# Kernel tuning notes

Measured on AMD Instinct MI355X. Metric: run time of the kernel, lower is better.

Reference implementation:

```python
import jax, jax.numpy as jnp
import numpy as np

EMB_DIM = 1024
N_HEAD = 16
HEAD_DIM = EMB_DIM // N_HEAD


def setup_inputs() -> dict:
    key = jax.random.key(0)
    kx, kq, kk, kv, ko = jax.random.split(key, 5)
    B, S = 4, 2048
    x = jax.random.normal(kx, (B, S, EMB_DIM), dtype=jnp.float32)
    attention_mask = jnp.ones((B, S), dtype=jnp.int32)
    s = 1.0 / np.sqrt(EMB_DIM)
    w_q = jax.random.normal(kq, (EMB_DIM, EMB_DIM), dtype=jnp.float32) * s
    w_k = jax.random.normal(kk, (EMB_DIM, EMB_DIM), dtype=jnp.float32) * s
    w_v = jax.random.normal(kv, (EMB_DIM, EMB_DIM), dtype=jnp.float32) * s
    w_o = jax.random.normal(ko, (EMB_DIM, EMB_DIM), dtype=jnp.float32) * s
    return {"x": x, "attention_mask": attention_mask,
            "w_q": w_q, "w_k": w_k, "w_v": w_v, "w_o": w_o}


def reference(x, attention_mask, w_q, w_k, w_v, w_o):
    B, S, _ = x.shape
    scale = 1.0 / np.sqrt(HEAD_DIM)
    # projections; nn.Linear computes x @ W^T
    def split_heads(t):
        return t.reshape(B, S, N_HEAD, HEAD_DIM).transpose(0, 2, 1, 3)  # [B,H,S,D]
    q = split_heads(x @ w_q.T)
    k = split_heads(x @ w_k.T)
    v = split_heads(x @ w_v.T)
    scores = jnp.einsum('bhqd,bhkd->bhqk', q, k) * scale  # [B,H,S,S]
    pad_mask = (attention_mask == 0)[:, None, None, :]          # [B,1,1,S]
    causal = jnp.triu(jnp.ones((S, S), dtype=bool), k=1)[None, None]  # [1,1,S,S]
    combined = pad_mask | causal
    scores = jnp.where(combined, -jnp.inf, scores)
    attn = jax.nn.softmax(scores, axis=-1)
    out = jnp.einsum('bhqk,bhkd->bhqd', attn, v)
    out = out.transpose(0, 2, 1, 3).reshape(B, S, EMB_DIM)
    return out @ w_o.T
```

## Files before the change

### kernel.cpp

```cpp
#include <hip/hip_runtime.h>

typedef __bf16 bf16x8 __attribute__((ext_vector_type(8)));
typedef float f32x4 __attribute__((ext_vector_type(4)));

#define LOG2E 1.4426950408889634f
#define NEGC (-12.0f * LOG2E)

__device__ inline unsigned short f2bf(float f) {
  unsigned int u = __builtin_bit_cast(unsigned int, f);
  u += 0x7fff + ((u >> 16) & 1);
  return (unsigned short)(u >> 16);
}

__device__ inline void async16(const void* g, void* l) {
  __builtin_amdgcn_global_load_lds(
      (__attribute__((address_space(1))) void*)(g),
      (__attribute__((address_space(3))) void*)(l), 16, 0, 0);
}

__global__ __launch_bounds__(256) void cast_all(
    const float* __restrict__ x, const float* __restrict__ w0,
    const float* __restrict__ w1, const float* __restrict__ w2,
    const float* __restrict__ w3, unsigned short* __restrict__ xb,
    unsigned short* __restrict__ ob ) {
  int id = blockIdx.x;
  const float* in;
  unsigned short* out;
  int boff;
  if (id < 8192) { in = x; out = xb; boff = id; }
  else {
    int w = (id - 8192) >> 10; boff = (id - 8192) & 1023;
    switch (w) { case 0: in = w0; break; case 1: in = w1; break;
                 case 2: in = w2; break; default: in = w3; }
    out = ob + (long)w * 1048576;
  }
  int i = (boff * 256 + threadIdx.x) * 4;
  float4 v = *(const float4*)(in + i);
  ushort4 o;
  o.x = f2bf(v.x); o.y = f2bf(v.y); o.z = f2bf(v.z); o.w = f2bf(v.w);
  *(ushort4*)(out + i) = o;
}

#define BM 128
#define BN 128
#define BK 32

__global__ __launch_bounds__(256, 3) void gemm_bt(
    const unsigned short* __restrict__ A, const unsigned short* __restrict__ W,
    void* __restrict__ out, int M, int N, int K, int mode) {
  __shared__ unsigned short SM[BM * BK + BN * BK];
  unsigned short* As = SM;
  unsigned short* Ws = SM + BM * BK;
  int tid = threadIdx.x;
  int lane = tid & 63, wid = tid >> 6;
  int wm = wid >> 1, wn = wid & 1;
  int l15 = lane & 15, quad = lane >> 4;
  int m0 = (blockIdx.x & 63) * BM, n0 = (blockIdx.x >> 6) * BN;

  f32x4 acc[4][4] = {};

  int srow = tid >> 2;
  int scol = (tid & 3) * 8;
  const unsigned short* Ag = A + (long)(m0 + srow) * K + scol;
  const unsigned short* Wg = W + (long)(n0 + srow) * K + scol;
  char* AsB = (char*)As + wid * 1024;
  char* WsB = (char*)Ws + wid * 1024;

  for (int kt = 0; kt < K; kt += BK) {
    __syncthreads();
    async16(Ag + kt, AsB);
    async16(Ag + kt + (long)64 * K, AsB + 4096);
    async16(Wg + kt, WsB);
    async16(Wg + kt + (long)64 * K, WsB + 4096);
    __syncthreads();
    bf16x8 af[4], wf[4];
#pragma unroll
    for (int t = 0; t < 4; t++)
      af[t] = *(const bf16x8*)(As + (wm * 64 + t * 16 + l15) * BK + quad * 8);
#pragma unroll
    for (int t = 0; t < 4; t++)
      wf[t] = *(const bf16x8*)(Ws + (wn * 64 + t * 16 + l15) * BK + quad * 8);
#pragma unroll
    for (int i = 0; i < 4; i++)
#pragma unroll
      for (int j = 0; j < 4; j++)
        acc[i][j] = __builtin_amdgcn_mfma_f32_16x16x32_bf16(af[i], wf[j], acc[i][j], 0, 0, 0);
  }

  if (mode == 0) {
    float* Cf = (float*)out;
#pragma unroll
    for (int i = 0; i < 4; i++) {
      int row = m0 + wm * 64 + i * 16 + quad * 4;
#pragma unroll
      for (int j = 0; j < 4; j++) {
        int col = n0 + wn * 64 + j * 16 + l15;
#pragma unroll
        for (int r = 0; r < 4; r++)
          Cf[(long)(row + r) * N + col] = acc[i][j][r];
      }
    }
  } else {
    unsigned short* Cb = (unsigned short*)out;
    int which = n0 >> 10;
    if (which == 2) {
#pragma unroll
      for (int i = 0; i < 4; i++)
#pragma unroll
        for (int j = 0; j < 4; j++) {
          int m = m0 + wm * 64 + i * 16 + quad * 4;
          int n = n0 + wn * 64 + j * 16 + l15;
          int nn = n & 1023;
          int b = m >> 11, s = m & 2047;
          int h = nn >> 6, d = nn & 63;
          ushort4 pk;
          pk.x = f2bf(acc[i][j][0]); pk.y = f2bf(acc[i][j][1]);
          pk.z = f2bf(acc[i][j][2]); pk.w = f2bf(acc[i][j][3]);
          *(ushort4*)(&Cb[16777216 + (((long)((b * 16 + h) * 64 + d)) << 11) + s]) = pk;
        }
    } else {
      float scale = (which == 0) ? 0.125f : 1.0f;
      int h0 = (n0 & 1023) >> 6;
      unsigned short* Es = SM;
#pragma unroll
      for (int qr = 0; qr < 4; qr++) {
        __syncthreads();
        if (wm == (qr >> 1)) {
#pragma unroll
          for (int ii = 0; ii < 2; ii++) {
            int i = (qr & 1) * 2 + ii;
#pragma unroll
            for (int j = 0; j < 4; j++)
#pragma unroll
              for (int r = 0; r < 4; r++) {
                int rr = (i & 1) * 16 + quad * 4 + r;
                Es[rr * 136 + wn * 64 + j * 16 + l15] = f2bf(acc[i][j][r] * scale);
              }
          }
        }
        __syncthreads();
#pragma unroll
        for (int p = 0; p < 2; p++) {
          int pair = p * 32 + (tid >> 3);
          int rq = pair >> 1;
          int head = pair & 1, c8 = tid & 7;
          uint4 v = *(const uint4*)(&Es[rq * 136 + head * 64 + c8 * 8]);
          int m = m0 + qr * 32 + rq;
          int b = m >> 11, s = m & 2047;
          int h = h0 + head;
          long idx = (long)which * 8388608 +
                     ((long)((b * 16 + h) * 2048 + s)) * 64 + c8 * 8;
          *(uint4*)(&Cb[idx]) = v;
        }
      }
    }
  }
}

#define BQ 128
#define BKV 64
#define PSTR 76

__global__ __launch_bounds__(256, 3) void attn(
    const unsigned short* __restrict__ Q, const unsigned short* __restrict__ Kt,
    const unsigned short* __restrict__ VT, const int* __restrict__ am,
    unsigned short* __restrict__ O) {
  __shared__ unsigned short QPs[BQ * PSTR];
  __shared__ unsigned short Ks[2][BKV * PSTR];
  const int S = 2048, D = 64;
  int tid = threadIdx.x, lane = tid & 63, wid = tid >> 6;
  int l15 = lane & 15, quad = lane >> 4;

  int id = blockIdx.x;
  int s = id >> 8;
  int r = id & 255;
  int bh = r & 63;
  int c = r >> 6;
  int qt;
  switch (s) { case 0: qt = 15 - c; break; case 1: qt = 8 + c; break;
               case 2: qt = 7 - c; break; default: qt = c; }
  int q0 = qt * BQ;
  int b = bh >> 4, h = bh & 15;
  const unsigned short* Qg = Q + (long)bh * S * D;
  const unsigned short* Kg = Kt + (long)bh * S * D;
  const unsigned short* Vg = VT + (long)bh * D * S;
  const int* amg = am + b * S;

  int row0 = tid >> 3, col0 = (tid & 7) * 8;
  int row1 = 32 + (tid >> 3), col1 = col0;

#pragma unroll
  for (int rr = 0; rr < 4; rr++) {
    int cc = rr * 256 + tid;
    int row = cc >> 3, col = (cc & 7) * 8;
    *(uint4*)(&QPs[row * PSTR + col]) = *(const uint4*)(Qg + (long)(q0 + row) * D + col);
  }

  uint4 kreg0 = *(const uint4*)(Kg + (long)row0 * D + col0);
  uint4 kreg1 = *(const uint4*)(Kg + (long)row1 * D + col1);

  __syncthreads();
  bf16x8 qf[2][2];
#pragma unroll
  for (int i = 0; i < 2; i++)
#pragma unroll
    for (int kk = 0; kk < 2; kk++)
      qf[i][kk] = *(const bf16x8*)(&QPs[(wid * 32 + i * 16 + l15) * PSTR + kk * 32 + quad * 8]);

  *(uint4*)(&Ks[0][row0 * PSTR + col0]) = kreg0;
  *(uint4*)(&Ks[0][row1 * PSTR + col1]) = kreg1;
  kreg0 = *(const uint4*)(Kg + (long)(BKV + row0) * D + col0);
  kreg1 = *(const uint4*)(Kg + (long)(BKV + row1) * D + col1);
  __syncthreads();

  f32x4 o_acc[2][4] = {};
  float lsum[2][4] = {};

  int tFull = q0 >> 6;
  int nt = tFull + 2;
  for (int t = 0; t < nt; t++) {
    int s0 = t * BKV;
    int cur = t & 1, nxt = cur ^ 1;

    *(uint4*)(&Ks[nxt][row0 * PSTR + col0]) = kreg0;
    *(uint4*)(&Ks[nxt][row1 * PSTR + col1]) = kreg1;

    int mvj[4];
#pragma unroll
    for (int j = 0; j < 4; j++) mvj[j] = amg[s0 + j * 16 + l15];

    f32x4 sacc[2][4] = {};
#pragma unroll
    for (int kk = 0; kk < 2; kk++) {
      bf16x8 kf[4];
#pragma unroll
      for (int j = 0; j < 4; j++)
        kf[j] = *(const bf16x8*)(&Ks[cur][(j * 16 + l15) * PSTR + kk * 32 + quad * 8]);
      __builtin_amdgcn_s_setprio(1);
#pragma unroll
      for (int i = 0; i < 2; i++)
#pragma unroll
        for (int j = 0; j < 4; j++)
          sacc[i][j] = __builtin_amdgcn_mfma_f32_16x16x32_bf16(qf[i][kk], kf[j], sacc[i][j], 0, 0, 0);
      __builtin_amdgcn_s_setprio(0);
    }

    __syncthreads();

    {
      long s0n = (long)(t + 2) * BKV; if (s0n > S - BKV) s0n = S - BKV;
      kreg0 = *(const uint4*)(Kg + (s0n + row0) * D + col0);
      kreg1 = *(const uint4*)(Kg + (s0n + row1) * D + col1);
    }

    bf16x8 vf[2][4];
#pragma unroll
    for (int kk = 0; kk < 2; kk++)
#pragma unroll
      for (int j = 0; j < 4; j++)
        vf[kk][j] = *(const bf16x8*)(Vg + (long)(j * 16 + l15) * S + s0 + kk * 32 + quad * 8);

    float fb[4];
#pragma unroll
    for (int j = 0; j < 4; j++) fb[j] = mvj[j] ? NEGC : -1e38f;

    if (t < tFull) {
#pragma unroll
      for (int i = 0; i < 2; i++)
#pragma unroll
        for (int rr = 0; rr < 4; rr++) {
          int prow = (wid * 32 + i * 16 + quad * 4 + rr) * PSTR;
          float rs = 0.f;
#pragma unroll
          for (int j = 0; j < 4; j++) {
            float p = __builtin_amdgcn_exp2f(fmaf(sacc[i][j][rr], LOG2E, fb[j]));
            unsigned int u = __builtin_bit_cast(unsigned int, p);
            QPs[prow + j * 16 + l15] = (unsigned short)(u >> 16);
            rs += __builtin_bit_cast(float, u & 0xffff0000u);
          }
          lsum[i][rr] += rs;
        }
    } else {
#pragma unroll
      for (int i = 0; i < 2; i++)
#pragma unroll
        for (int rr = 0; rr < 4; rr++) {
          int row = q0 + wid * 32 + i * 16 + quad * 4 + rr;
          int prow = (wid * 32 + i * 16 + quad * 4 + rr) * PSTR;
          float rs = 0.f;
#pragma unroll
          for (int j = 0; j < 4; j++) {
            int col = s0 + j * 16 + l15;
            float fbe = (col > row) ? -1e38f : fb[j];
            float p = __builtin_amdgcn_exp2f(fmaf(sacc[i][j][rr], LOG2E, fbe));
            unsigned int u = __builtin_bit_cast(unsigned int, p);
            QPs[prow + j * 16 + l15] = (unsigned short)(u >> 16);
            rs += __builtin_bit_cast(float, u & 0xffff0000u);
          }
          lsum[i][rr] += rs;
        }
    }

#pragma unroll
    for (int kk = 0; kk < 2; kk++) {
      bf16x8 pf[2];
#pragma unroll
      for (int i = 0; i < 2; i++)
        pf[i] = *(const bf16x8*)(&QPs[(wid * 32 + i * 16 + l15) * PSTR + kk * 32 + quad * 8]);
      __builtin_amdgcn_s_setprio(1);
#pragma unroll
      for (int i = 0; i < 2; i++)
#pragma unroll
        for (int j = 0; j < 4; j++)
          o_acc[i][j] = __builtin_amdgcn_mfma_f32_16x16x32_bf16(pf[i], vf[kk][j], o_acc[i][j], 0, 0, 0);
      __builtin_amdgcn_s_setprio(0);
    }
  }

#pragma unroll
  for (int i = 0; i < 2; i++)
#pragma unroll
    for (int rr = 0; rr < 4; rr++) {
      float tsum = lsum[i][rr];
      tsum += __shfl_xor(tsum, 1, 64);
      tsum += __shfl_xor(tsum, 2, 64);
      tsum += __shfl_xor(tsum, 4, 64);
      tsum += __shfl_xor(tsum, 8, 64);
      float inv = 1.0f / tsum;
      int prow = (wid * 32 + i * 16 + quad * 4 + rr) * PSTR;
#pragma unroll
      for (int j = 0; j < 4; j++)
        QPs[prow + j * 16 + l15] = f2bf(o_acc[i][j][rr] * inv);
    }
  __syncthreads();
#pragma unroll
  for (int rr = 0; rr < 4; rr++) {
    int cc = rr * 256 + tid;
    int row = cc >> 3, col = (cc & 7) * 8;
    uint4 v = *(const uint4*)(&QPs[row * PSTR + col]);
    long gm = (long)b * S + q0 + row;
    *(uint4*)(&O[gm * 1024 + h * 64 + col]) = v;
  }
}

extern "C" void kernel_launch(void* const* d_in, const int* in_sizes, int n_in,
                              void* d_out, int out_size, void* d_ws, size_t ws_size,
                              hipStream_t stream) {
  const float* x  = (const float*)d_in[0];
  const int*   am = (const int*)d_in[1];
  const float* wq = (const float*)d_in[2];
  const float* wk = (const float*)d_in[3];
  const float* wv = (const float*)d_in[4];
  const float* wo = (const float*)d_in[5];
  float* out = (float*)d_out;

  const int S = 2048, E = 1024, Bb = 4, H = 16;
  const int M = Bb * S;

  char* ws = (char*)d_ws;
  unsigned short* xb  = (unsigned short*)ws;
  unsigned short* wqb = (unsigned short*)(ws + 16777216);
  unsigned short* wob = wqb + 3 * 1048576;
  unsigned short* Qb  = (unsigned short*)(ws + 25165824);
  unsigned short* Ob  = Qb + 25165824;

  cast_all<<<12288, 256, 0, stream>>>(x, wq, wk, wv, wo, xb, wqb);

  gemm_bt<<<dim3((3 * E / BN) * (M / BM)), 256, 0, stream>>>(xb, wqb, Qb, M, 3 * E, E, 4);
  attn<<<dim3(1024), 256, 0, stream>>>(Qb, Qb + 8388608, Qb + 16777216, am, Ob);
  gemm_bt<<<dim3((E / BN) * (M / BM)), 256, 0, stream>>>(Ob, wob, out, M, E, E, 0);
}
```

Baseline: 275.7 us.

## Transpose QK^T MFMA, stage V in LDS, pack P stores, ballot mask

Swaps the MFMA operand order in the score computation so each lane holds four consecutive key columns for one query row. P can then be written to LDS as packed 64-bit stores instead of scalar 16-bit stores. The row-sum reduction shrinks to two cross-quad shuffles, and the per-column mask loads become a single per-tile load plus ballot. V tiles are now staged through LDS alongside a single-buffered K tile with register prefetch, instead of being read straight from global memory into registers. In exchange, each iteration carries two barriers because K/V double-buffering is dropped.

```diff
diff --git a/kernel.cpp b/kernel.cpp
--- a/kernel.cpp
+++ b/kernel.cpp
@@ -166,7 +166,8 @@
     const unsigned short* __restrict__ VT, const int* __restrict__ am,
     unsigned short* __restrict__ O) {
   __shared__ unsigned short QPs[BQ * PSTR];
-  __shared__ unsigned short Ks[2][BKV * PSTR];
+  __shared__ unsigned short Ks[BKV * PSTR];
+  __shared__ unsigned short Vs[64 * PSTR];
   const int S = 2048, D = 64;
   int tid = threadIdx.x, lane = tid & 63, wid = tid >> 6;
   int l15 = lane & 15, quad = lane >> 4;
@@ -198,6 +199,8 @@
 
   uint4 kreg0 = *(const uint4*)(Kg + (long)row0 * D + col0);
   uint4 kreg1 = *(const uint4*)(Kg + (long)row1 * D + col1);
+  uint4 vreg0 = *(const uint4*)(Vg + (long)row0 * S + col0);
+  uint4 vreg1 = *(const uint4*)(Vg + (long)row1 * S + col1);
 
   __syncthreads();
   bf16x8 qf[2][2];
@@ -207,27 +210,29 @@
     for (int kk = 0; kk < 2; kk++)
       qf[i][kk] = *(const bf16x8*)(&QPs[(wid * 32 + i * 16 + l15) * PSTR + kk * 32 + quad * 8]);
 
-  *(uint4*)(&Ks[0][row0 * PSTR + col0]) = kreg0;
-  *(uint4*)(&Ks[0][row1 * PSTR + col1]) = kreg1;
-  kreg0 = *(const uint4*)(Kg + (long)(BKV + row0) * D + col0);
-  kreg1 = *(const uint4*)(Kg + (long)(BKV + row1) * D + col1);
-  __syncthreads();
-
   f32x4 o_acc[2][4] = {};
-  float lsum[2][4] = {};
+  float lsum[2] = {};
 
   int tFull = q0 >> 6;
   int nt = tFull + 2;
   for (int t = 0; t < nt; t++) {
     int s0 = t * BKV;
-    int cur = t & 1, nxt = cur ^ 1;
-
-    *(uint4*)(&Ks[nxt][row0 * PSTR + col0]) = kreg0;
-    *(uint4*)(&Ks[nxt][row1 * PSTR + col1]) = kreg1;
-
-    int mvj[4];
-#pragma unroll
-    for (int j = 0; j < 4; j++) mvj[j] = amg[s0 + j * 16 + l15];
+    __syncthreads();
+    *(uint4*)(&Ks[row0 * PSTR + col0]) = kreg0;
+    *(uint4*)(&Ks[row1 * PSTR + col1]) = kreg1;
+    *(uint4*)(&Vs[row0 * PSTR + col0]) = vreg0;
+    *(uint4*)(&Vs[row1 * PSTR + col1]) = vreg1;
+    __syncthreads();
+
+    {
+      long s0n = (t + 1) * BKV; if (s0n > S - BKV) s0n = S - BKV;
+      kreg0 = *(const uint4*)(Kg + (s0n + row0) * D + col0);
+      kreg1 = *(const uint4*)(Kg + (s0n + row1) * D + col1);
+      vreg0 = *(const uint4*)(Vg + (long)row0 * S + s0n + col0);
+      vreg1 = *(const uint4*)(Vg + (long)row1 * S + s0n + col1);
+    }
+
+    int amv = amg[s0 + lane];
 
     f32x4 sacc[2][4] = {};
 #pragma unroll
@@ -235,103 +240,99 @@
       bf16x8 kf[4];
 #pragma unroll
       for (int j = 0; j < 4; j++)
-        kf[j] = *(const bf16x8*)(&Ks[cur][(j * 16 + l15) * PSTR + kk * 32 + quad * 8]);
+        kf[j] = *(const bf16x8*)(&Ks[(j * 16 + l15) * PSTR + kk * 32 + quad * 8]);
       __builtin_amdgcn_s_setprio(1);
 #pragma unroll
       for (int i = 0; i < 2; i++)
 #pragma unroll
         for (int j = 0; j < 4; j++)
-          sacc[i][j] = __builtin_amdgcn_mfma_f32_16x16x32_bf16(qf[i][kk], kf[j], sacc[i][j], 0, 0, 0);
+          sacc[i][j] = __builtin_amdgcn_mfma_f32_16x16x32_bf16(kf[j], qf[i][kk], sacc[i][j], 0, 0, 0);
       __builtin_amdgcn_s_setprio(0);
     }
 
-    __syncthreads();
-
-    {
-      long s0n = (long)(t + 2) * BKV; if (s0n > S - BKV) s0n = S - BKV;
-      kreg0 = *(const uint4*)(Kg + (s0n + row0) * D + col0);
-      kreg1 = *(const uint4*)(Kg + (s0n + row1) * D + col1);
-    }
-
-    bf16x8 vf[2][4];
-#pragma unroll
-    for (int kk = 0; kk < 2; kk++)
-#pragma unroll
-      for (int j = 0; j < 4; j++)
-        vf[kk][j] = *(const bf16x8*)(Vg + (long)(j * 16 + l15) * S + s0 + kk * 32 + quad * 8);
-
-    float fb[4];
-#pragma unroll
-    for (int j = 0; j < 4; j++) fb[j] = mvj[j] ? NEGC : -1e38f;
+    unsigned long long bal = __ballot(amv != 0);
 
     if (t < tFull) {
 #pragma unroll
-      for (int i = 0; i < 2; i++)
-#pragma unroll
-        for (int rr = 0; rr < 4; rr++) {
-          int prow = (wid * 32 + i * 16 + quad * 4 + rr) * PSTR;
-          float rs = 0.f;
-#pragma unroll
-          for (int j = 0; j < 4; j++) {
-            float p = __builtin_amdgcn_exp2f(fmaf(sacc[i][j][rr], LOG2E, fb[j]));
-            unsigned int u = __builtin_bit_cast(unsigned int, p);
-            QPs[prow + j * 16 + l15] = (unsigned short)(u >> 16);
-            rs += __builtin_bit_cast(float, u & 0xffff0000u);
+      for (int i = 0; i < 2; i++) {
+        float rs = 0.f;
+#pragma unroll
+        for (int j = 0; j < 4; j++) {
+          unsigned nib = (unsigned)(bal >> (j * 16 + quad * 4)) & 15u;
+          unsigned v[4];
+#pragma unroll
+          for (int r = 0; r < 4; r++) {
+            float fbe = ((nib >> r) & 1) ? NEGC : -1e38f;
+            float p = __builtin_amdgcn_exp2f(fmaf(sacc[i][j][r], LOG2E, fbe));
+            v[r] = __builtin_bit_cast(unsigned, p) & 0xffff0000u;
+            rs += __builtin_bit_cast(float, v[r]);
           }
-          lsum[i][rr] += rs;
-        }
+          uint2 pk;
+          pk.x = (v[0] >> 16) | v[1];
+          pk.y = (v[2] >> 16) | v[3];
+          *(uint2*)(&QPs[(wid * 32 + i * 16 + l15) * PSTR + j * 16 + quad * 4]) = pk;
+        }
+        lsum[i] += rs;
+      }
     } else {
 #pragma unroll
-      for (int i = 0; i < 2; i++)
-#pragma unroll
-        for (int rr = 0; rr < 4; rr++) {
-          int row = q0 + wid * 32 + i * 16 + quad * 4 + rr;
-          int prow = (wid * 32 + i * 16 + quad * 4 + rr) * PSTR;
-          float rs = 0.f;
-#pragma unroll
-          for (int j = 0; j < 4; j++) {
-            int col = s0 + j * 16 + l15;
-            float fbe = (col > row) ? -1e38f : fb[j];
-            float p = __builtin_amdgcn_exp2f(fmaf(sacc[i][j][rr], LOG2E, fbe));
-            unsigned int u = __builtin_bit_cast(unsigned int, p);
-            QPs[prow + j * 16 + l15] = (unsigned short)(u >> 16);
-            rs += __builtin_bit_cast(float, u & 0xffff0000u);
+      for (int i = 0; i < 2; i++) {
+        int qrow = q0 + wid * 32 + i * 16 + l15;
+        float rs = 0.f;
+#pragma unroll
+        for (int j = 0; j < 4; j++) {
+          unsigned nib = (unsigned)(bal >> (j * 16 + quad * 4)) & 15u;
+          unsigned v[4];
+#pragma unroll
+          for (int r = 0; r < 4; r++) {
+            int kv = s0 + j * 16 + quad * 4 + r;
+            float fbe = (((nib >> r) & 1) && kv <= qrow) ? NEGC : -1e38f;
+            float p = __builtin_amdgcn_exp2f(fmaf(sacc[i][j][r], LOG2E, fbe));
+            v[r] = __builtin_bit_cast(unsigned, p) & 0xffff0000u;
+            rs += __builtin_bit_cast(float, v[r]);
           }
-          lsum[i][rr] += rs;
-        }
+          uint2 pk;
+          pk.x = (v[0] >> 16) | v[1];
+          pk.y = (v[2] >> 16) | v[3];
+          *(uint2*)(&QPs[(wid * 32 + i * 16 + l15) * PSTR + j * 16 + quad * 4]) = pk;
+        }
+        lsum[i] += rs;
+      }
     }
 
 #pragma unroll
     for (int kk = 0; kk < 2; kk++) {
-      bf16x8 pf[2];
+      bf16x8 pf[2], vf[4];
 #pragma unroll
       for (int i = 0; i < 2; i++)
         pf[i] = *(const bf16x8*)(&QPs[(wid * 32 + i * 16 + l15) * PSTR + kk * 32 + quad * 8]);
+#pragma unroll
+      for (int j = 0; j < 4; j++)
+        vf[j] = *(const bf16x8*)(&Vs[(j * 16 + l15) * PSTR + kk * 32 + quad * 8]);
       __builtin_amdgcn_s_setprio(1);
 #pragma unroll
       for (int i = 0; i < 2; i++)
 #pragma unroll
         for (int j = 0; j < 4; j++)
-          o_acc[i][j] = __builtin_amdgcn_mfma_f32_16x16x32_bf16(pf[i], vf[kk][j], o_acc[i][j], 0, 0, 0);
+          o_acc[i][j] = __builtin_amdgcn_mfma_f32_16x16x32_bf16(pf[i], vf[j], o_acc[i][j], 0, 0, 0);
       __builtin_amdgcn_s_setprio(0);
     }
   }
 
 #pragma unroll
-  for (int i = 0; i < 2; i++)
+  for (int i = 0; i < 2; i++) {
+    float ts = lsum[i];
+    ts += __shfl_xor(ts, 16, 64);
+    ts += __shfl_xor(ts, 32, 64);
 #pragma unroll
     for (int rr = 0; rr < 4; rr++) {
-      float tsum = lsum[i][rr];
-      tsum += __shfl_xor(tsum, 1, 64);
-      tsum += __shfl_xor(tsum, 2, 64);
-      tsum += __shfl_xor(tsum, 4, 64);
-      tsum += __shfl_xor(tsum, 8, 64);
-      float inv = 1.0f / tsum;
+      float inv = 1.0f / __shfl(ts, quad * 4 + rr, 64);
       int prow = (wid * 32 + i * 16 + quad * 4 + rr) * PSTR;
 #pragma unroll
       for (int j = 0; j < 4; j++)
         QPs[prow + j * 16 + l15] = f2bf(o_acc[i][j][rr] * inv);
     }
+  }
   __syncthreads();
 #pragma unroll
   for (int rr = 0; rr < 4; rr++) {
```

After: 241.5 us. 1.14x faster.
